# Performance work log

Hardware: AMD Instinct MI355X
Metric: run time of the kernel (lower is better)

The kernel has to match this reference:

```python
import jax, jax.numpy as jnp
import numpy as np
from jax import lax


def setup_inputs() -> dict:
    key = jax.random.key(0)
    k1, k2 = jax.random.split(key)
    x = jax.random.normal(k1, (32, 128, 64, 64), dtype=jnp.float32)
    # learned kernel, original shape (k, k, in_channels, out_channels)
    K = jax.random.normal(k2, (3, 3, 128, 256), dtype=jnp.float32) * 0.05
    return {"x": x, "K": K}


def reference(x, K):
    stride, padding = 1, 1
    kh = K.shape[0]
    C = K.shape[2]
    O = K.shape[3]
    H = x.shape[-1]
    P = H + 2 * padding
    out_size = (P - kh) // stride + 1
    # Original pairs x-patches flattened as (C, kh, kw) with K flattened
    # row-major as (kh, kw, C), matched purely by flat index. Equivalent to a
    # standard conv with the weight buffer reinterpreted as (C, kh, kw, O):
    W = K.reshape(-1, O).reshape(C, kh, kh, O).transpose(3, 0, 1, 2)  # (O,C,kh,kw)
    out = lax.conv_general_dilated(
        x, W,
        window_strides=(stride, stride),
        padding=[(padding, padding), (padding, padding)],
        dimension_numbers=("NCHW", "OIHW", "NCHW"),
    )  # (B, O, out_size, out_size)
    # Original loop uses range(0, P - kh, stride) (missing +1): when
    # (P - kh) % stride == 0 the last output row/col is never written (stays 0).
    n_filled = -(-(P - kh) // stride)  # ceil((P-kh)/stride), static
    if n_filled < out_size:
        out = out.at[:, :, n_filled:, :].set(0.0)
        out = out.at[:, :, :, n_filled:].set(0.0)
    return out
```

## Files before the change

### kernel.cpp

```cpp
#include <hip/hip_runtime.h>
#include <hip/hip_bf16.h>

typedef __attribute__((ext_vector_type(8))) short bf16x8;
typedef __attribute__((ext_vector_type(4))) float f32x4;

#define CIN   128
#define HW    64
#define OUTC  256

#define BP_OFF     33554432ULL
#define ZP_OFF     34144256ULL
#define WS_NEEDED  34148352ULL

#define SB  __builtin_amdgcn_s_barrier()
#define SCB __builtin_amdgcn_sched_barrier(0)
#define WAITV(N) asm volatile("s_waitcnt vmcnt(" #N ")" ::: "memory")
#define MFMA(a, b, c) __builtin_amdgcn_mfma_f32_16x16x32_bf16(a, b, c, 0, 0, 0)

__global__ __launch_bounds__(256) void conv_prep(const float* __restrict__ X,
                                                 const float* __restrict__ Kw,
                                                 __hip_bfloat16* __restrict__ Xt,
                                                 __hip_bfloat16* __restrict__ Bp,
                                                 __hip_bfloat16* __restrict__ zp) {
    const int blk = blockIdx.x;
    if (blk < 2048) {
        __shared__ __hip_bfloat16 L[64][136];
        const int b = blk >> 6;
        const int y = blk & 63;
        const int x = threadIdx.x & 63;
        const int c0 = (threadIdx.x >> 6) * 32;
        const float* src = X + (((long)(b * CIN + c0) * HW + y) * HW + x);
        #pragma unroll
        for (int j = 0; j < 32; j += 2) {
            float v0 = src[(long)j * (HW * HW)];
            float v1 = src[(long)(j + 1) * (HW * HW)];
            __hip_bfloat162 p;
            p.x = __float2bfloat16(v0);
            p.y = __float2bfloat16(v1);
            *reinterpret_cast<__hip_bfloat162*>(&L[x][c0 + j]) = p;
        }
        __syncthreads();
        __hip_bfloat16* dst = Xt + (long)blk * (64 * 128);
        #pragma unroll
        for (int it = 0; it < 4; ++it) {
            int G = it * 256 + threadIdx.x;
            int xx = G >> 4, g = G & 15;
            bf16x8 v = *reinterpret_cast<const bf16x8*>(&L[xx][g * 8]);
            *reinterpret_cast<bf16x8*>(&dst[(long)G * 8]) = v;
        }
    } else if (blk < 2112) {
        for (int idx = (blk - 2048) * 256 + threadIdx.x; idx < 294912; idx += 64 * 256) {
            int c  = idx & 127;
            int n  = (idx >> 7) & 255;
            int ij = idx >> 15;
            Bp[idx] = __float2bfloat16(Kw[((c * 9 + ij) << 8) + n]);
        }
    } else {
        *reinterpret_cast<float4*>((char*)zp + threadIdx.x * 16) = float4{0.f, 0.f, 0.f, 0.f};
    }
}

__global__ __launch_bounds__(512, 2) void conv_igemm6(
    const __hip_bfloat16* __restrict__ Xt,
    const __hip_bfloat16* __restrict__ Bp,
    const __hip_bfloat16* __restrict__ zp,
    float* __restrict__ out)
{
    __shared__ __hip_bfloat16 As[4][256 * 32];
    __shared__ __hip_bfloat16 Bs[4][256 * 32];

    const int tid  = threadIdx.x;
    const int wv   = tid >> 6;
    const int lane = tid & 63;
    const int l16  = lane & 15;
    const int d16  = lane >> 4;
    const int wr   = wv >> 2;
    const int wc   = wv & 3;

    const int bid   = blockIdx.x;
    const int mtile = (bid & 7) * 64 + (bid >> 3);
    const int b  = mtile >> 4;
    const int y0 = (mtile & 15) * 4;

    const int srow = lane >> 2;
    const int sg   = lane & 3;

    f32x4 acc[8][4] = {};

    const int r0  = wv * 32 + srow;
    const int r1  = r0 + 16;
    const int G0  = (sg - (r0 >> 1)) & 3;
    const int G1  = (sg - (r1 >> 1)) & 3;
    const int xr0 = r0 & 63, xr1 = r1 & 63;
    const int yy0 = y0 + (r0 >> 6), yy1 = y0 + (r1 >> 6);
    const __hip_bfloat16* pA0 = Xt + (((long)b * 4096 + yy0 * 64 + xr0) * 128 + G0 * 8);
    const __hip_bfloat16* pA1 = Xt + (((long)b * 4096 + yy1 * 64 + xr1) * 128 + G1 * 8);
    const __hip_bfloat16* pB0 = Bp + ((long)r0 * 128 + G0 * 8);
    const __hip_bfloat16* pB1 = Bp + ((long)r1 * 128 + G1 * 8);
    const int ldsOff0 = (wv * 32) * 32;
    const int ldsOff1 = (wv * 32 + 16) * 32;

    auto stage = [&](int S) {
        const int ij = S >> 2;
        const int c0 = (S & 3) * 32;
        const int di = ij / 3 - 1;
        const int dj = ij % 3 - 1;
        const long offA = (long)(di * 64 + dj) * 128 + c0;
        const bool ok0 = ((unsigned)(xr0 + dj) < 64u) && ((unsigned)(yy0 + di) < 64u);
        const bool ok1 = ((unsigned)(xr1 + dj) < 64u) && ((unsigned)(yy1 + di) < 64u);
        const __hip_bfloat16* gA0 = ok0 ? pA0 + offA : zp + c0;
        const __hip_bfloat16* gA1 = ok1 ? pA1 + offA : zp + c0;
        __hip_bfloat16* ldsA = &As[S & 3][0];
        __builtin_amdgcn_global_load_lds(
            (const __attribute__((address_space(1))) void*)gA0,
            (__attribute__((address_space(3))) void*)(ldsA + ldsOff0), 16, 0, 0);
        __builtin_amdgcn_global_load_lds(
            (const __attribute__((address_space(1))) void*)gA1,
            (__attribute__((address_space(3))) void*)(ldsA + ldsOff1), 16, 0, 0);
        const long offB = (long)ij * 32768 + c0;
        __hip_bfloat16* ldsB = &Bs[S & 3][0];
        __builtin_amdgcn_global_load_lds(
            (const __attribute__((address_space(1))) void*)(pB0 + offB),
            (__attribute__((address_space(3))) void*)(ldsB + ldsOff0), 16, 0, 0);
        __builtin_amdgcn_global_load_lds(
            (const __attribute__((address_space(1))) void*)(pB1 + offB),
            (__attribute__((address_space(3))) void*)(ldsB + ldsOff1), 16, 0, 0);
    };

    stage(0); stage(1); stage(2);
    WAITV(8);
    SCB; SB;

    #pragma unroll
    for (int H = 0; H < 36; ++H) {
        const int RB = H & 3;
        bf16x8 Af[8], Bf[4];
        #pragma unroll
        for (int mi = 0; mi < 8; ++mi) {
            const int m = wr * 128 + mi * 16 + l16;
            const int s = (d16 + (m >> 1)) & 3;
            Af[mi] = *reinterpret_cast<const bf16x8*>(&As[RB][m * 32 + s * 8]);
        }
        #pragma unroll
        for (int ni = 0; ni < 4; ++ni) {
            const int n = wc * 64 + ni * 16 + l16;
            const int s = (d16 + (n >> 1)) & 3;
            Bf[ni] = *reinterpret_cast<const bf16x8*>(&Bs[RB][n * 32 + s * 8]);
        }
        if (H < 33) stage(H + 3);
        if (H < 33)       WAITV(8);
        else if (H == 33) WAITV(4);
        else if (H == 34) WAITV(0);
        SCB; SB;
        __builtin_amdgcn_s_setprio(1);
        #pragma unroll
        for (int ni = 0; ni < 4; ++ni)
            #pragma unroll
            for (int mi = 0; mi < 8; ++mi)
                acc[mi][ni] = MFMA(Af[mi], Bf[ni], acc[mi][ni]);
        __builtin_amdgcn_s_setprio(0);
        SCB; SB;
    }

    #pragma unroll
    for (int mi = 0; mi < 8; ++mi) {
        const int m  = wr * 128 + mi * 16 + d16 * 4;
        const int x0 = m & 63;
        const int y  = y0 + (m >> 6);
        #pragma unroll
        for (int ni = 0; ni < 4; ++ni) {
            const int o = wc * 64 + ni * 16 + l16;
            float4 v;
            v.x = acc[mi][ni][0];
            v.y = acc[mi][ni][1];
            v.z = acc[mi][ni][2];
            v.w = acc[mi][ni][3];
            if (y == HW - 1) { v.x = v.y = v.z = v.w = 0.f; }
            if (x0 + 3 == HW - 1) v.w = 0.f;
            *reinterpret_cast<float4*>(
                out + ((long)(b * OUTC + o) * 4096 + y * 64 + x0)) = v;
        }
    }
}

__global__ __launch_bounds__(256) void conv_igemm_bf16(
    const float* __restrict__ X, const float* __restrict__ Kw, float* __restrict__ out) {
    __shared__ __hip_bfloat16 As[128][40];
    __shared__ __hip_bfloat16 Bs[128][40];
    const int tid = threadIdx.x, wave = tid >> 6, lane = tid & 63;
    const int l16 = lane & 15, d16 = lane >> 4;
    const int m_base = blockIdx.x * 128;
    const int b = m_base >> 12, y0 = (m_base & 4095) >> 6;
    const int n_base = blockIdx.y * 128;
    const int wm = (wave >> 1) * 64, wn = (wave & 1) * 64;
    f32x4 acc[4][4] = {};
    const int smm = tid & 127, ccb = tid >> 7;
    const int sx = smm & 63, syr = smm >> 6;
    for (int ij = 0; ij < 9; ++ij) {
        const int di = ij / 3 - 1, dj = ij % 3 - 1;
        const int xp = sx + dj, yp = y0 + syr + di;
        const bool ok = ((unsigned)xp < 64u) && ((unsigned)yp < 64u);
        const long xbase = (((long)b * CIN) * HW + yp) * HW + xp;
        for (int c0 = 0; c0 < CIN; c0 += 32) {
            for (int cc = ccb; cc < 32; cc += 2) {
                float v = ok ? X[xbase + (long)(c0 + cc) * 4096] : 0.f;
                As[smm][cc] = __float2bfloat16(v);
                Bs[smm][cc] = __float2bfloat16(Kw[((c0 + cc) * 9 + ij) * OUTC + n_base + smm]);
            }
            __syncthreads();
            bf16x8 afrag[4], bfrag[4];
            for (int mi = 0; mi < 4; ++mi)
                afrag[mi] = *reinterpret_cast<const bf16x8*>(&As[wm + mi * 16 + l16][d16 * 8]);
            for (int ni = 0; ni < 4; ++ni)
                bfrag[ni] = *reinterpret_cast<const bf16x8*>(&Bs[wn + ni * 16 + l16][d16 * 8]);
            for (int mi = 0; mi < 4; ++mi)
                for (int ni = 0; ni < 4; ++ni)
                    acc[mi][ni] = __builtin_amdgcn_mfma_f32_16x16x32_bf16(
                        afrag[mi], bfrag[ni], acc[mi][ni], 0, 0, 0);
            __syncthreads();
        }
    }
    for (int mi = 0; mi < 4; ++mi)
        for (int ni = 0; ni < 4; ++ni)
            for (int r = 0; r < 4; ++r) {
                const int mm = wm + mi * 16 + d16 * 4 + r;
                const int nn = wn + ni * 16 + l16;
                const int y = y0 + (mm >> 6), x = mm & 63, o = n_base + nn;
                float v = acc[mi][ni][r];
                if (y == 63 || x == 63) v = 0.f;
                out[(((long)b * OUTC + o) * HW + y) * HW + x] = v;
            }
}

extern "C" void kernel_launch(void* const* d_in, const int* in_sizes, int n_in,
                              void* d_out, int out_size, void* d_ws, size_t ws_size,
                              hipStream_t stream) {
    const float* X  = (const float*)d_in[0];
    const float* Kw = (const float*)d_in[1];
    float* out = (float*)d_out;

    if (ws_size >= WS_NEEDED) {
        char* ws = (char*)d_ws;
        __hip_bfloat16* Xt = (__hip_bfloat16*)ws;
        __hip_bfloat16* Bp = (__hip_bfloat16*)(ws + BP_OFF);
        __hip_bfloat16* zp = (__hip_bfloat16*)(ws + ZP_OFF);
        conv_prep<<<dim3(2113), dim3(256), 0, stream>>>(X, Kw, Xt, Bp, zp);
        conv_igemm6<<<dim3(512), dim3(512), 0, stream>>>(Xt, Bp, zp, out);
    } else {
        conv_igemm_bf16<<<dim3(1024, 2), dim3(256), 0, stream>>>(X, Kw, out);
    }
}
```

Measured before the change: 109.1 us.

## Block channels into 32-wide chunks in prepacked activation and weight layouts

```diff
diff --git a/kernel.cpp b/kernel.cpp
--- a/kernel.cpp
+++ b/kernel.cpp
@@ -19,8 +19,8 @@
 
 __global__ __launch_bounds__(256) void conv_prep(const float* __restrict__ X,
                                                  const float* __restrict__ Kw,
-                                                 __hip_bfloat16* __restrict__ Xt,
-                                                 __hip_bfloat16* __restrict__ Bp,
+                                                 __hip_bfloat16* __restrict__ Xt2,
+                                                 __hip_bfloat16* __restrict__ Bp2,
                                                  __hip_bfloat16* __restrict__ zp) {
     const int blk = blockIdx.x;
     if (blk < 2048) {
@@ -40,29 +40,31 @@
             *reinterpret_cast<__hip_bfloat162*>(&L[x][c0 + j]) = p;
         }
         __syncthreads();
-        __hip_bfloat16* dst = Xt + (long)blk * (64 * 128);
-        #pragma unroll
-        for (int it = 0; it < 4; ++it) {
-            int G = it * 256 + threadIdx.x;
-            int xx = G >> 4, g = G & 15;
-            bf16x8 v = *reinterpret_cast<const bf16x8*>(&L[xx][g * 8]);
-            *reinterpret_cast<bf16x8*>(&dst[(long)G * 8]) = v;
+        const int xx = threadIdx.x >> 2;
+        const int g  = threadIdx.x & 3;
+        #pragma unroll
+        for (int cc = 0; cc < 4; ++cc) {
+            bf16x8 v = *reinterpret_cast<const bf16x8*>(&L[xx][cc * 32 + g * 8]);
+            long dst = (((long)(b * 4 + cc) * 64 + y) * 64 + xx) * 32 + g * 8;
+            *reinterpret_cast<bf16x8*>(&Xt2[dst]) = v;
         }
     } else if (blk < 2112) {
-        for (int idx = (blk - 2048) * 256 + threadIdx.x; idx < 294912; idx += 64 * 256) {
-            int c  = idx & 127;
-            int n  = (idx >> 7) & 255;
-            int ij = idx >> 15;
-            Bp[idx] = __float2bfloat16(Kw[((c * 9 + ij) << 8) + n]);
+        for (int i = (blk - 2048) * 256 + threadIdx.x; i < 294912; i += 64 * 256) {
+            int c32 = i & 31;
+            int n   = (i >> 5) & 255;
+            int cc  = (i >> 13) & 3;
+            int ij  = i >> 15;
+            int c   = cc * 32 + c32;
+            Bp2[i] = __float2bfloat16(Kw[(c * 9 + ij) * 256 + n]);
         }
     } else {
         *reinterpret_cast<float4*>((char*)zp + threadIdx.x * 16) = float4{0.f, 0.f, 0.f, 0.f};
     }
 }
 
-__global__ __launch_bounds__(512, 2) void conv_igemm6(
-    const __hip_bfloat16* __restrict__ Xt,
-    const __hip_bfloat16* __restrict__ Bp,
+__global__ __launch_bounds__(512, 2) void conv_igemm7(
+    const __hip_bfloat16* __restrict__ Xt2,
+    const __hip_bfloat16* __restrict__ Bp2,
     const __hip_bfloat16* __restrict__ zp,
     float* __restrict__ out)
 {
@@ -93,23 +95,25 @@
     const int G1  = (sg - (r1 >> 1)) & 3;
     const int xr0 = r0 & 63, xr1 = r1 & 63;
     const int yy0 = y0 + (r0 >> 6), yy1 = y0 + (r1 >> 6);
-    const __hip_bfloat16* pA0 = Xt + (((long)b * 4096 + yy0 * 64 + xr0) * 128 + G0 * 8);
-    const __hip_bfloat16* pA1 = Xt + (((long)b * 4096 + yy1 * 64 + xr1) * 128 + G1 * 8);
-    const __hip_bfloat16* pB0 = Bp + ((long)r0 * 128 + G0 * 8);
-    const __hip_bfloat16* pB1 = Bp + ((long)r1 * 128 + G1 * 8);
+    const __hip_bfloat16* pA0 = Xt2 + (((long)b * 16384 + yy0 * 64 + xr0) * 32 + G0 * 8);
+    const __hip_bfloat16* pA1 = Xt2 + (((long)b * 16384 + yy1 * 64 + xr1) * 32 + G1 * 8);
+    const __hip_bfloat16* pB0 = Bp2 + ((long)r0 * 32 + G0 * 8);
+    const __hip_bfloat16* pB1 = Bp2 + ((long)r1 * 32 + G1 * 8);
+    const __hip_bfloat16* zp0 = zp + G0 * 8;
+    const __hip_bfloat16* zp1 = zp + G1 * 8;
     const int ldsOff0 = (wv * 32) * 32;
     const int ldsOff1 = (wv * 32 + 16) * 32;
 
     auto stage = [&](int S) {
         const int ij = S >> 2;
-        const int c0 = (S & 3) * 32;
+        const int cc = S & 3;
         const int di = ij / 3 - 1;
         const int dj = ij % 3 - 1;
-        const long offA = (long)(di * 64 + dj) * 128 + c0;
+        const long offA = ((long)cc * 4096 + di * 64 + dj) * 32;
         const bool ok0 = ((unsigned)(xr0 + dj) < 64u) && ((unsigned)(yy0 + di) < 64u);
         const bool ok1 = ((unsigned)(xr1 + dj) < 64u) && ((unsigned)(yy1 + di) < 64u);
-        const __hip_bfloat16* gA0 = ok0 ? pA0 + offA : zp + c0;
-        const __hip_bfloat16* gA1 = ok1 ? pA1 + offA : zp + c0;
+        const __hip_bfloat16* gA0 = ok0 ? pA0 + offA : zp0;
+        const __hip_bfloat16* gA1 = ok1 ? pA1 + offA : zp1;
         __hip_bfloat16* ldsA = &As[S & 3][0];
         __builtin_amdgcn_global_load_lds(
             (const __attribute__((address_space(1))) void*)gA0,
@@ -117,7 +121,7 @@
         __builtin_amdgcn_global_load_lds(
             (const __attribute__((address_space(1))) void*)gA1,
             (__attribute__((address_space(3))) void*)(ldsA + ldsOff1), 16, 0, 0);
-        const long offB = (long)ij * 32768 + c0;
+        const long offB = (long)(ij * 4 + cc) * 8192;
         __hip_bfloat16* ldsB = &Bs[S & 3][0];
         __builtin_amdgcn_global_load_lds(
             (const __attribute__((address_space(1))) void*)(pB0 + offB),
@@ -241,11 +245,11 @@
 
     if (ws_size >= WS_NEEDED) {
         char* ws = (char*)d_ws;
-        __hip_bfloat16* Xt = (__hip_bfloat16*)ws;
-        __hip_bfloat16* Bp = (__hip_bfloat16*)(ws + BP_OFF);
-        __hip_bfloat16* zp = (__hip_bfloat16*)(ws + ZP_OFF);
-        conv_prep<<<dim3(2113), dim3(256), 0, stream>>>(X, Kw, Xt, Bp, zp);
-        conv_igemm6<<<dim3(512), dim3(512), 0, stream>>>(Xt, Bp, zp, out);
+        __hip_bfloat16* Xt2 = (__hip_bfloat16*)ws;
+        __hip_bfloat16* Bp2 = (__hip_bfloat16*)(ws + BP_OFF);
+        __hip_bfloat16* zp  = (__hip_bfloat16*)(ws + ZP_OFF);
+        conv_prep<<<dim3(2113), dim3(256), 0, stream>>>(X, Kw, Xt2, Bp2, zp);
+        conv_igemm7<<<dim3(512), dim3(512), 0, stream>>>(Xt2, Bp2, zp, out);
     } else {
         conv_igemm_bf16<<<dim3(1024, 2), dim3(256), 0, stream>>>(X, Kw, out);
     }
```

Result: faster. 105.3 us (-3.4%).
